# Optimization experiments

Measured on AMD Instinct MI355X. Metric: run time of the kernel, lower is better.

The kernel has to match this reference:

```python
import jax, jax.numpy as jnp
import numpy as np

EMBED = 1024
HEADS = 16
HEAD_DIM = EMBED // HEADS

def setup_inputs() -> dict:
    key = jax.random.key(0)
    ks = jax.random.split(key, 9)
    N, Q, K = 2, 2048, 2048
    queries = jax.random.normal(ks[0], (N, Q, EMBED), dtype=jnp.float32)
    keys_ = jax.random.normal(ks[1], (N, K, EMBED), dtype=jnp.float32)
    values = jax.random.normal(ks[2], (N, K, EMBED), dtype=jnp.float32)
    mask = jax.random.randint(ks[3], (N, 1, Q, K), 0, 2, dtype=jnp.int32)
    s = 1.0 / np.sqrt(EMBED)
    Wq = jax.random.normal(ks[4], (EMBED, EMBED), dtype=jnp.float32) * s
    Wk = jax.random.normal(ks[5], (EMBED, EMBED), dtype=jnp.float32) * s
    Wv = jax.random.normal(ks[6], (EMBED, EMBED), dtype=jnp.float32) * s
    Wo = jax.random.normal(ks[7], (EMBED, EMBED), dtype=jnp.float32) * s
    bo = jax.random.normal(ks[8], (EMBED,), dtype=jnp.float32) * s
    return {"queries": queries, "keys": keys_, "values": values, "mask": mask,
            "Wq": Wq, "Wk": Wk, "Wv": Wv, "Wo": Wo, "bo": bo}

def reference(queries, keys, values, mask, Wq, Wk, Wv, Wo, bo):
    N, Qlen, _ = queries.shape
    Klen = keys.shape[1]
    # Linear projections (torch Linear: x @ W.T), then split heads
    q = (queries @ Wq.T).reshape(N, Qlen, HEADS, HEAD_DIM)
    k = (keys @ Wk.T).reshape(N, Klen, HEADS, HEAD_DIM)
    v = (values @ Wv.T).reshape(N, Klen, HEADS, HEAD_DIM)
    energy = jnp.einsum('nqhd,nkhd->nhqk', q, k)  # [N,H,Q,K]
    energy = jnp.where(mask == 0, jnp.float32(-1e20), energy)
    # NOTE: original scales by sqrt(embed_size), not sqrt(head_dim)
    attention = jax.nn.softmax(energy / jnp.sqrt(jnp.float32(EMBED)), axis=3)
    out = jnp.einsum('nhqk,nkhd->nqhd', attention, v).reshape(N, Qlen, EMBED)
    return out @ Wo.T + bo
```

## Files before the change

### kernel.cpp

```cpp
#include <hip/hip_runtime.h>
#include <stdint.h>
#include <stddef.h>

typedef __attribute__((ext_vector_type(8)))  short bf16x8;
typedef __attribute__((ext_vector_type(2)))  float f32x2;
typedef __attribute__((ext_vector_type(4)))  float f32x4;
typedef __attribute__((ext_vector_type(16))) float f32x16;
typedef __attribute__((ext_vector_type(4)))  float float4v;
typedef __attribute__((ext_vector_type(4)))  int   int4v;

#define DEV static __device__ __forceinline__

static constexpr int EMBED  = 1024;
static constexpr int HEADS  = 16;
static constexpr int SEQ    = 2048;

DEV short f2bf(float f) {
  union { float f; unsigned u; } x; x.f = f;
  unsigned r = x.u + 0x7fffu + ((x.u >> 16) & 1u);
  return (short)(r >> 16);
}

DEV int cvtpk(float a, float b) {
  int r; asm("v_cvt_pk_bf16_f32 %0, %1, %2" : "=v"(r) : "v"(a), "v"(b)); return r;
}

DEV float fexp2(float x) { float r; asm("v_exp_f32 %0, %1" : "=v"(r) : "v"(x)); return r; }

#define MFMA16(a,b,c) __builtin_amdgcn_mfma_f32_16x16x32_bf16((a),(b),(c),0,0,0)
#define MFMA32(a,b,c) __builtin_amdgcn_mfma_f32_32x32x16_bf16((a),(b),(c),0,0,0)
#define GLDS(g,l) __builtin_amdgcn_global_load_lds( \
    (const __attribute__((address_space(1))) void*)(g), \
    (__attribute__((address_space(3))) void*)(l), 16, 0, 0)
#define SBAR0() __builtin_amdgcn_sched_barrier(0)
#define ZERO16 {0,0,0,0,0,0,0,0,0,0,0,0,0,0,0,0}
#define ROT3(x) ((x) == 2 ? 0 : (x) + 1)


struct CvtArgs { const float* src[7]; short* dst[7]; int n[7]; };

__global__ void cvt_bf16(CvtArgs a) {
  const int task = blockIdx.y;
  const int i = (blockIdx.x * 256 + threadIdx.x) * 8;
  if (i >= a.n[task]) return;
  const float4v* s = (const float4v*)(a.src[task] + i);
  float4v x = s[0], y = s[1];
  bf16x8 o;
  o[0] = f2bf(x[0]); o[1] = f2bf(x[1]); o[2] = f2bf(x[2]); o[3] = f2bf(x[3]);
  o[4] = f2bf(y[0]); o[5] = f2bf(y[1]); o[6] = f2bf(y[2]); o[7] = f2bf(y[3]);
  *(bf16x8*)(a.dst[task] + i) = o;
}

__global__ void maskpack(const int* __restrict__ m, unsigned long long* __restrict__ out) {
  const int gw = (blockIdx.x * 256 + threadIdx.x) >> 6;
  const int l  = threadIdx.x & 63;
  const int n = gw >> 16, kvblk = (gw >> 11) & 31, q = gw & 2047;
  int v = m[((size_t)n * SEQ + q) * SEQ + kvblk * 64 + l];
  unsigned long long b = __ballot(v != 0);
  if (l == 0) out[((size_t)n * 32 + kvblk) * SEQ + q] = b;
}

template<int MODE>
DEV void gemm_core(const int vv, const short* __restrict__ A, const short* __restrict__ B,
                   short* __restrict__ Cb, float* __restrict__ Cf,
                   const float* __restrict__ bias, short* As, short* Bs)
{
  const int t = threadIdx.x;
  const int l = t & 63, w = t >> 6;
  const int lr = l & 15, lh = l >> 4;
  const int m0 = (vv >> 3) * 128, n0 = (vv & 7) * 128;
  const int wr = w >> 1, wc = w & 1;
  f32x4 acc[4][4] = {};

  const int rA = t >> 2, cA = (t & 3) * 8;
  const short* gA  = A + (size_t)(m0 + rA) * 1024 + cA;
  const short* gA2 = gA + (size_t)64 * 1024;
  const short* gB  = B + (size_t)(n0 + rA) * 1024 + cA;
  const short* gB2 = gB + (size_t)64 * 1024;

  GLDS(gA,       As + w * 512);
  GLDS(gA2,      As + 2048 + w * 512);
  GLDS(gB,       Bs + w * 512);
  GLDS(gB2,      Bs + 2048 + w * 512);
  SBAR0();
  GLDS(gA + 32,  As + 4096 + w * 512);
  GLDS(gA2 + 32, As + 4096 + 2048 + w * 512);
  GLDS(gB + 32,  Bs + 4096 + w * 512);
  GLDS(gB2 + 32, Bs + 4096 + 2048 + w * 512);
  SBAR0();

  int cb = 0, sb = 2;
  #pragma unroll 1
  for (int it = 0; it < 32; ++it) {
    if (it < 31) { asm volatile("s_waitcnt vmcnt(4)" ::: "memory"); }
    else         { asm volatile("s_waitcnt vmcnt(0)" ::: "memory"); }
    SBAR0();
    __builtin_amdgcn_s_barrier();
    SBAR0();
    if (it < 30) {
      const int kt = (it + 2) * 32;
      GLDS(gA + kt,  As + sb * 4096 + w * 512);
      GLDS(gA2 + kt, As + sb * 4096 + 2048 + w * 512);
      GLDS(gB + kt,  Bs + sb * 4096 + w * 512);
      GLDS(gB2 + kt, Bs + sb * 4096 + 2048 + w * 512);
      SBAR0();
    }

    const short* as = As + cb * 4096;
    const short* bs = Bs + cb * 4096;
    bf16x8 af[4], bq[4];
    #pragma unroll
    for (int i = 0; i < 4; ++i)
      af[i] = *(const bf16x8*)&as[(wr * 64 + i * 16 + lr) * 32 + lh * 8];
    #pragma unroll
    for (int i = 0; i < 4; ++i)
      bq[i] = *(const bf16x8*)&bs[(wc * 64 + i * 16 + lr) * 32 + lh * 8];
    #pragma unroll
    for (int mi = 0; mi < 4; ++mi)
      #pragma unroll
      for (int ni = 0; ni < 4; ++ni)
        acc[mi][ni] = MFMA16(af[mi], bq[ni], acc[mi][ni]);

    SBAR0();
    cb = ROT3(cb); sb = ROT3(sb);
  }

  #pragma unroll
  for (int mi = 0; mi < 4; ++mi)
    #pragma unroll
    for (int ni = 0; ni < 4; ++ni)
      #pragma unroll
      for (int r = 0; r < 4; ++r) {
        const int m = m0 + wr * 64 + mi * 16 + lh * 4 + r;
        const int e = n0 + wc * 64 + ni * 16 + lr;
        const float v = acc[mi][ni][r];
        const int nb = m >> 11, s = m & 2047, hh = e >> 6, d = e & 63;
        if (MODE == 0) {
          Cb[(((size_t)(nb * HEADS + hh)) * SEQ + s) * 64 + d] = f2bf(v);
        } else if (MODE == 2) {
          Cb[(((size_t)(nb * HEADS + hh)) * SEQ + s) * 64 + (d ^ ((s & 7) << 3))] = f2bf(v);
        } else {
          Cb[(((size_t)(nb * HEADS + hh)) * 32 + (s >> 6)) * 4096 + d * 64 +
             ((s & 63) ^ ((d & 7) << 3))] = f2bf(v);
        }
      }
}

__global__ __launch_bounds__(256, 3)
void gemm_qkv(const short* __restrict__ Ab, const short* __restrict__ Bb,
              short* __restrict__ Qp, short* __restrict__ Kp, short* __restrict__ VTp)
{
  __shared__ short As[3][4096];
  __shared__ short Bs[3][4096];
  const int lin = blockIdx.x;
  const int s = lin >> 8, j = lin & 255;
  const int vv = (j & 7) * 32 + (j >> 3);
  const short* A = Ab + (size_t)s * 4194304;
  const short* B = Bb + (size_t)s * 1048576;
  if (s == 0)      gemm_core<0>(vv, A, B, Qp,  nullptr, nullptr, &As[0][0], &Bs[0][0]);
  else if (s == 1) gemm_core<2>(vv, A, B, Kp,  nullptr, nullptr, &As[0][0], &Bs[0][0]);
  else             gemm_core<3>(vv, A, B, VTp, nullptr, nullptr, &As[0][0], &Bs[0][0]);
}

__global__ __launch_bounds__(256, 2)
void gemm_out(const short* __restrict__ A, const short* __restrict__ B,
              float* __restrict__ Cf, const float* __restrict__ bias)
{
  __shared__ short AsArr[3][2048];
  __shared__ short BsArr[3][4096];
  short* As = &AsArr[0][0];
  short* Bs = &BsArr[0][0];
  const int lin = blockIdx.x;
  const int vv = (lin & 7) * 64 + (lin >> 3);
  const int t = threadIdx.x;
  const int l = t & 63, w = t >> 6;
  const int lr = l & 15, lh = l >> 4;
  const int m0 = (vv >> 3) * 64, n0 = (vv & 7) * 128;
  const int wr = w >> 1, wc = w & 1;
  f32x4 acc[2][4] = {};

  const int rA = t >> 2, cA = (t & 3) * 8;
  const short* gA  = A + (size_t)(m0 + rA) * 1024 + cA;
  const short* gB  = B + (size_t)(n0 + rA) * 1024 + cA;
  const short* gB2 = gB + (size_t)64 * 1024;

  GLDS(gA,       As + w * 512);
  GLDS(gB,       Bs + w * 512);
  GLDS(gB2,      Bs + 2048 + w * 512);
  SBAR0();
  GLDS(gA + 32,  As + 2048 + w * 512);
  GLDS(gB + 32,  Bs + 4096 + w * 512);
  GLDS(gB2 + 32, Bs + 4096 + 2048 + w * 512);
  SBAR0();

  int cb = 0, sb = 2;
  #pragma unroll 1
  for (int it = 0; it < 32; ++it) {
    if (it < 31) { asm volatile("s_waitcnt vmcnt(3)" ::: "memory"); }
    else         { asm volatile("s_waitcnt vmcnt(0)" ::: "memory"); }
    SBAR0();
    __builtin_amdgcn_s_barrier();
    SBAR0();
    if (it < 30) {
      const int kt = (it + 2) * 32;
      GLDS(gA + kt,  As + sb * 2048 + w * 512);
      GLDS(gB + kt,  Bs + sb * 4096 + w * 512);
      GLDS(gB2 + kt, Bs + sb * 4096 + 2048 + w * 512);
      SBAR0();
    }

    const short* as = As + cb * 2048;
    const short* bs = Bs + cb * 4096;
    bf16x8 af[2], bq[4];
    #pragma unroll
    for (int i = 0; i < 2; ++i)
      af[i] = *(const bf16x8*)&as[(wr * 32 + i * 16 + lr) * 32 + lh * 8];
    #pragma unroll
    for (int i = 0; i < 4; ++i)
      bq[i] = *(const bf16x8*)&bs[(wc * 64 + i * 16 + lr) * 32 + lh * 8];
    #pragma unroll
    for (int mi = 0; mi < 2; ++mi)
      #pragma unroll
      for (int ni = 0; ni < 4; ++ni)
        acc[mi][ni] = MFMA16(af[mi], bq[ni], acc[mi][ni]);

    SBAR0();
    cb = ROT3(cb); sb = ROT3(sb);
  }

  #pragma unroll
  for (int mi = 0; mi < 2; ++mi)
    #pragma unroll
    for (int ni = 0; ni < 4; ++ni)
      #pragma unroll
      for (int r = 0; r < 4; ++r) {
        const int m = m0 + wr * 32 + mi * 16 + lh * 4 + r;
        const int e = n0 + wc * 64 + ni * 16 + lr;
        Cf[(size_t)m * EMBED + e] = acc[mi][ni][r] + bias[e];
      }
}

__global__ __launch_bounds__(256, 2)
void attn256(const short* __restrict__ Qp, const short* __restrict__ Kp,
             const short* __restrict__ VTp, const unsigned long long* __restrict__ MbT,
             short* __restrict__ Aout)
{
  __shared__ short lds[2][8192];

  const int t = threadIdx.x, l = t & 63, w = t >> 6;
  const int lq = l & 31, hi = l >> 5;
  const int lin = blockIdx.x;
  const int vv = (lin & 7) * 64 + (lin >> 3);
  const int hl = vv >> 4, qb = vv & 15;
  const int n = hl >> 4, h = hl & 15;
  const int q0 = qb * 128;
  const int myq = q0 + w * 32 + lq;
  const size_t hb = (size_t)(n * HEADS + h) * SEQ * 64;
  const short* Qh = Qp + hb;
  const float SCL = 0.045084220027780106f;

  bf16x8 qf[4];
  #pragma unroll
  for (int ks = 0; ks < 4; ++ks)
    qf[ks] = *(const bf16x8*)(Qh + (size_t)myq * 64 + ks * 16 + hi * 8);

  const short ONE = (short)0x3F80;
  const bf16x8 onesv = {ONE, ONE, ONE, ONE, ONE, ONE, ONE, ONE};
  const f32x16 zerov = ZERO16;

  f32x16 acco[2] = { ZERO16, ZERO16 };
  f32x16 accl = ZERO16;

  const short* kgp = Kp + hb + w * 1024 + l * 8;
  const short* vgp = VTp + hb + w * 1024 + l * 8;
  const unsigned long long* mp = MbT + (size_t)n * (32 * SEQ) + myq;

  unsigned long long mw = *mp; mp += SEQ;
  {
    GLDS(kgp,       &lds[0][w * 1024]);
    GLDS(kgp + 512, &lds[0][w * 1024 + 512]);
    GLDS(vgp,       &lds[0][4096 + w * 1024]);
    GLDS(vgp + 512, &lds[0][4096 + w * 1024 + 512]);
    kgp += 4096; vgp += 4096;
  }

  #pragma unroll 1
  for (int tt = 0; tt < 32; ++tt) {
    unsigned long long mw_next = 0;
    if (tt < 31) {
      mw_next = *mp; mp += SEQ;
      SBAR0();
      const int nb = (tt + 1) & 1;
      GLDS(kgp,       &lds[nb][w * 1024]);
      GLDS(kgp + 512, &lds[nb][w * 1024 + 512]);
      GLDS(vgp,       &lds[nb][4096 + w * 1024]);
      GLDS(vgp + 512, &lds[nb][4096 + w * 1024 + 512]);
      kgp += 4096; vgp += 4096;
      asm volatile("s_waitcnt vmcnt(5)" ::: "memory");
      SBAR0();
    } else {
      asm volatile("s_waitcnt vmcnt(0)" ::: "memory");
      SBAR0();
    }
    __builtin_amdgcn_s_barrier();
    SBAR0();

    const short* Ks  = &lds[tt & 1][0];
    const short* VTs = &lds[tt & 1][4096];

    #pragma unroll
    for (int half = 0; half < 2; ++half) {
      f32x16 sacc;
      __builtin_amdgcn_s_setprio(1);
      #pragma unroll
      for (int ks = 0; ks < 4; ++ks) {
        const int d = ks * 16 + hi * 8;
        bf16x8 kf = *(const bf16x8*)&Ks[(half * 32 + lq) * 64 + (d ^ ((lq & 7) << 3))];
        sacc = MFMA32(kf, qf[ks], ks == 0 ? zerov : sacc);
      }
      __builtin_amdgcn_s_setprio(0);
      const unsigned mmw = ~(unsigned)(mw >> (half * 32 + hi * 4));
      float p[16];
      #pragma unroll
      for (int r = 0; r < 16; ++r) {
        const int idx = (r & 3) + 8 * (r >> 2);
        union { int i; float f; } b;
        b.i = __builtin_amdgcn_sbfe(mmw, idx, 1) & 0xC3480000;
        p[r] = fexp2(__builtin_fmaf(sacc[r], SCL, b.f));
      }
      bf16x8 pf[2];
      #pragma unroll
      for (int kb = 0; kb < 2; ++kb) {
        int x1 = cvtpk(p[kb * 8 + 0], p[kb * 8 + 1]);
        int y1 = cvtpk(p[kb * 8 + 4], p[kb * 8 + 5]);
        int x2 = cvtpk(p[kb * 8 + 2], p[kb * 8 + 3]);
        int y2 = cvtpk(p[kb * 8 + 6], p[kb * 8 + 7]);
        asm("v_permlane32_swap_b32 %0, %1" : "+v"(x1), "+v"(y1));
        asm("v_permlane32_swap_b32 %0, %1" : "+v"(x2), "+v"(y2));
        union { int w4[4]; bf16x8 v; } u;
        u.w4[0] = x1; u.w4[1] = x2; u.w4[2] = y1; u.w4[3] = y2;
        pf[kb] = u.v;
      }
      __builtin_amdgcn_s_setprio(1);
      accl = MFMA32(onesv, pf[0], accl);
      accl = MFMA32(onesv, pf[1], accl);
      #pragma unroll
      for (int dt = 0; dt < 2; ++dt) {
        const int d = dt * 32 + lq;
        #pragma unroll
        for (int kb = 0; kb < 2; ++kb) {
          const int kv = half * 32 + kb * 16 + hi * 8;
          bf16x8 vf = *(const bf16x8*)&VTs[d * 64 + (kv ^ ((d & 7) << 3))];
          acco[dt] = MFMA32(vf, pf[kb], acco[dt]);
        }
      }
      __builtin_amdgcn_s_setprio(0);
    }
    mw = mw_next;
    SBAR0();
    __builtin_amdgcn_s_barrier();
    SBAR0();
  }

  const float invs = 1.f / (accl[0] + 1e-30f);

  short* ot = &lds[0][0] + w * 2048;
  #pragma unroll
  for (int dt = 0; dt < 2; ++dt)
    #pragma unroll
    for (int r = 0; r < 16; ++r) {
      const int d = dt * 32 + (r & 3) + 8 * (r >> 2) + 4 * hi;
      ot[lq * 64 + (d ^ ((lq & 7) << 3))] = f2bf(acco[dt][r] * invs);
    }
  __syncthreads();

  const int qq = l >> 1, hb2 = l & 1;
  #pragma unroll
  for (int it = 0; it < 4; ++it) {
    const int didx = (hb2 * 32 + it * 8) ^ ((qq & 7) << 3);
    bf16x8 v = *(const bf16x8*)&ot[qq * 64 + didx];
    *(bf16x8*)&Aout[((size_t)(n * SEQ + q0 + w * 32 + qq)) * EMBED + h * 64 + hb2 * 32 + it * 8] = v;
  }
}

extern "C" void kernel_launch(void* const* d_in, const int* in_sizes, int n_in,
                              void* d_out, int out_size, void* d_ws, size_t ws_size,
                              hipStream_t stream) {
  (void)in_sizes; (void)n_in; (void)out_size;
  const float* queries = (const float*)d_in[0];
  const float* keys    = (const float*)d_in[1];
  const float* values  = (const float*)d_in[2];
  const int*   mask    = (const int*)d_in[3];
  const float* Wq      = (const float*)d_in[4];
  const float* Wk      = (const float*)d_in[5];
  const float* Wv      = (const float*)d_in[6];
  const float* Wo      = (const float*)d_in[7];
  const float* bo      = (const float*)d_in[8];

  const size_t NEED = (size_t)76 * 1024 * 1024;
  if (ws_size < NEED) return;

  char* ws = (char*)d_ws;
  short* qb   = (short*)(ws + 0);
  short* kb   = (short*)(ws + (8u << 20));
  short* vb   = (short*)(ws + (16u << 20));
  short* wqb  = (short*)(ws + (24u << 20));
  short* wkb  = (short*)(ws + (26u << 20));
  short* wvb  = (short*)(ws + (28u << 20));
  short* wob  = (short*)(ws + (30u << 20));
  unsigned long long* mbits = (unsigned long long*)(ws + (32u << 20));
  short* Qp   = (short*)(ws + (40u << 20));
  short* Kp   = (short*)(ws + (48u << 20));
  short* VTp  = (short*)(ws + (56u << 20));
  short* ao   = (short*)(ws + (64u << 20));

  const int NTOK = 2 * SEQ * EMBED;
  const int NW   = EMBED * EMBED;

  CvtArgs ca;
  ca.src[0] = queries; ca.dst[0] = qb;  ca.n[0] = NTOK;
  ca.src[1] = keys;    ca.dst[1] = kb;  ca.n[1] = NTOK;
  ca.src[2] = values;  ca.dst[2] = vb;  ca.n[2] = NTOK;
  ca.src[3] = Wq;      ca.dst[3] = wqb; ca.n[3] = NW;
  ca.src[4] = Wk;      ca.dst[4] = wkb; ca.n[4] = NW;
  ca.src[5] = Wv;      ca.dst[5] = wvb; ca.n[5] = NW;
  ca.src[6] = Wo;      ca.dst[6] = wob; ca.n[6] = NW;
  cvt_bf16<<<dim3(2048, 7), 256, 0, stream>>>(ca);

  maskpack<<<dim3(32768), 256, 0, stream>>>(mask, mbits);

  gemm_qkv<<<dim3(768), 256, 0, stream>>>(qb, wqb, Qp, Kp, VTp);

  attn256<<<dim3(512), 256, 0, stream>>>(Qp, Kp, VTp, mbits, ao);

  gemm_out<<<dim3(512), 256, 0, stream>>>(ao, wob, (float*)d_out, bo);
}
```

Before: 141.9 us.

## Fuse fp32-to-bf16 activation conversion into QKV GEMM loads

The QKV projection GEMM now reads fp32 activations straight from global memory into registers, packs them to bf16 and writes them to LDS itself. The separate conversion pass over queries, keys and values is dropped, so only the weights still go through the cvt kernel. This removes a full write and re-read of the bf16 activation copies. In exchange the A-operand path loses the async global-to-LDS load, reads twice as many bytes per tile, and needs an extra LDS barrier every iteration.

```diff
diff --git a/kernel.cpp b/kernel.cpp
--- a/kernel.cpp
+++ b/kernel.cpp
@@ -37,7 +37,7 @@
 #define ROT3(x) ((x) == 2 ? 0 : (x) + 1)
 
 
-struct CvtArgs { const float* src[7]; short* dst[7]; int n[7]; };
+struct CvtArgs { const float* src[4]; short* dst[4]; int n[4]; };
 
 __global__ void cvt_bf16(CvtArgs a) {
   const int task = blockIdx.y;
@@ -61,9 +61,8 @@
 }
 
 template<int MODE>
-DEV void gemm_core(const int vv, const short* __restrict__ A, const short* __restrict__ B,
-                   short* __restrict__ Cb, float* __restrict__ Cf,
-                   const float* __restrict__ bias, short* As, short* Bs)
+DEV void gemm_qkv_core(const int vv, const float* __restrict__ A, const short* __restrict__ B,
+                       short* __restrict__ Cb, short* As, short* Bs)
 {
   const int t = threadIdx.x;
   const int l = t & 63, w = t >> 6;
@@ -73,39 +72,71 @@
   f32x4 acc[4][4] = {};
 
   const int rA = t >> 2, cA = (t & 3) * 8;
-  const short* gA  = A + (size_t)(m0 + rA) * 1024 + cA;
-  const short* gA2 = gA + (size_t)64 * 1024;
+  const float* gA  = A + (size_t)(m0 + rA) * 1024 + cA;
+  const float* gA2 = gA + (size_t)64 * 1024;
   const short* gB  = B + (size_t)(n0 + rA) * 1024 + cA;
   const short* gB2 = gB + (size_t)64 * 1024;
 
-  GLDS(gA,       As + w * 512);
-  GLDS(gA2,      As + 2048 + w * 512);
+  short* wA  = As + t * 8;
+  short* wA2 = As + 2048 + t * 8;
+
+  float4v a0 = *(const float4v*)(gA);
+  float4v a1 = *(const float4v*)(gA + 4);
+  float4v a2 = *(const float4v*)(gA2);
+  float4v a3 = *(const float4v*)(gA2 + 4);
+  {
+    union { int w4[4]; bf16x8 v; } u1, u2;
+    u1.w4[0] = cvtpk(a0[0], a0[1]); u1.w4[1] = cvtpk(a0[2], a0[3]);
+    u1.w4[2] = cvtpk(a1[0], a1[1]); u1.w4[3] = cvtpk(a1[2], a1[3]);
+    u2.w4[0] = cvtpk(a2[0], a2[1]); u2.w4[1] = cvtpk(a2[2], a2[3]);
+    u2.w4[2] = cvtpk(a3[0], a3[1]); u2.w4[3] = cvtpk(a3[2], a3[3]);
+    *(bf16x8*)(wA)  = u1.v;
+    *(bf16x8*)(wA2) = u2.v;
+  }
+  SBAR0();
+  a0 = *(const float4v*)(gA + 32);
+  a1 = *(const float4v*)(gA + 36);
+  a2 = *(const float4v*)(gA2 + 32);
+  a3 = *(const float4v*)(gA2 + 36);
+  SBAR0();
   GLDS(gB,       Bs + w * 512);
   GLDS(gB2,      Bs + 2048 + w * 512);
-  SBAR0();
-  GLDS(gA + 32,  As + 4096 + w * 512);
-  GLDS(gA2 + 32, As + 4096 + 2048 + w * 512);
   GLDS(gB + 32,  Bs + 4096 + w * 512);
   GLDS(gB2 + 32, Bs + 4096 + 2048 + w * 512);
   SBAR0();
-
-  int cb = 0, sb = 2;
+  asm volatile("s_waitcnt vmcnt(0) lgkmcnt(0)" ::: "memory");
+  SBAR0();
+  __builtin_amdgcn_s_barrier();
+  SBAR0();
+
+  int cb = 0, sbA = 1, sbB = 2;
   #pragma unroll 1
   for (int it = 0; it < 32; ++it) {
-    if (it < 31) { asm volatile("s_waitcnt vmcnt(4)" ::: "memory"); }
-    else         { asm volatile("s_waitcnt vmcnt(0)" ::: "memory"); }
-    SBAR0();
-    __builtin_amdgcn_s_barrier();
-    SBAR0();
+    if (it > 0) {
+      if (it < 31) { asm volatile("s_waitcnt vmcnt(2)" ::: "memory"); }
+      else         { asm volatile("s_waitcnt vmcnt(0)" ::: "memory"); }
+      SBAR0();
+    }
+    if (it < 31) {
+      union { int w4[4]; bf16x8 v; } u1, u2;
+      u1.w4[0] = cvtpk(a0[0], a0[1]); u1.w4[1] = cvtpk(a0[2], a0[3]);
+      u1.w4[2] = cvtpk(a1[0], a1[1]); u1.w4[3] = cvtpk(a1[2], a1[3]);
+      u2.w4[0] = cvtpk(a2[0], a2[1]); u2.w4[1] = cvtpk(a2[2], a2[3]);
+      u2.w4[2] = cvtpk(a3[0], a3[1]); u2.w4[3] = cvtpk(a3[2], a3[3]);
+      *(bf16x8*)(wA  + sbA * 4096) = u1.v;
+      *(bf16x8*)(wA2 + sbA * 4096) = u2.v;
+      SBAR0();
+    }
     if (it < 30) {
       const int kt = (it + 2) * 32;
-      GLDS(gA + kt,  As + sb * 4096 + w * 512);
-      GLDS(gA2 + kt, As + sb * 4096 + 2048 + w * 512);
-      GLDS(gB + kt,  Bs + sb * 4096 + w * 512);
-      GLDS(gB2 + kt, Bs + sb * 4096 + 2048 + w * 512);
-      SBAR0();
-    }
-
+      a0 = *(const float4v*)(gA + kt);
+      a1 = *(const float4v*)(gA + kt + 4);
+      a2 = *(const float4v*)(gA2 + kt);
+      a3 = *(const float4v*)(gA2 + kt + 4);
+      GLDS(gB + kt,  Bs + sbB * 4096 + w * 512);
+      GLDS(gB2 + kt, Bs + sbB * 4096 + 2048 + w * 512);
+      SBAR0();
+    }
     const short* as = As + cb * 4096;
     const short* bs = Bs + cb * 4096;
     bf16x8 af[4], bq[4];
@@ -122,7 +153,11 @@
         acc[mi][ni] = MFMA16(af[mi], bq[ni], acc[mi][ni]);
 
     SBAR0();
-    cb = ROT3(cb); sb = ROT3(sb);
+    asm volatile("s_waitcnt lgkmcnt(0)" ::: "memory");
+    SBAR0();
+    __builtin_amdgcn_s_barrier();
+    SBAR0();
+    cb = ROT3(cb); sbA = ROT3(sbA); sbB = ROT3(sbB);
   }
 
   #pragma unroll
@@ -147,7 +182,8 @@
 }
 
 __global__ __launch_bounds__(256, 3)
-void gemm_qkv(const short* __restrict__ Ab, const short* __restrict__ Bb,
+void gemm_qkv(const float* __restrict__ Aq, const float* __restrict__ Ak,
+              const float* __restrict__ Av, const short* __restrict__ Bb,
               short* __restrict__ Qp, short* __restrict__ Kp, short* __restrict__ VTp)
 {
   __shared__ short As[3][4096];
@@ -155,11 +191,10 @@
   const int lin = blockIdx.x;
   const int s = lin >> 8, j = lin & 255;
   const int vv = (j & 7) * 32 + (j >> 3);
-  const short* A = Ab + (size_t)s * 4194304;
   const short* B = Bb + (size_t)s * 1048576;
-  if (s == 0)      gemm_core<0>(vv, A, B, Qp,  nullptr, nullptr, &As[0][0], &Bs[0][0]);
-  else if (s == 1) gemm_core<2>(vv, A, B, Kp,  nullptr, nullptr, &As[0][0], &Bs[0][0]);
-  else             gemm_core<3>(vv, A, B, VTp, nullptr, nullptr, &As[0][0], &Bs[0][0]);
+  if (s == 0)      gemm_qkv_core<0>(vv, Aq, B, Qp,  &As[0][0], &Bs[0][0]);
+  else if (s == 1) gemm_qkv_core<2>(vv, Ak, B, Kp,  &As[0][0], &Bs[0][0]);
+  else             gemm_qkv_core<3>(vv, Av, B, VTp, &As[0][0], &Bs[0][0]);
 }
 
 __global__ __launch_bounds__(256, 2)
@@ -401,12 +436,7 @@
   if (ws_size < NEED) return;
 
   char* ws = (char*)d_ws;
-  short* qb   = (short*)(ws + 0);
-  short* kb   = (short*)(ws + (8u << 20));
-  short* vb   = (short*)(ws + (16u << 20));
   short* wqb  = (short*)(ws + (24u << 20));
-  short* wkb  = (short*)(ws + (26u << 20));
-  short* wvb  = (short*)(ws + (28u << 20));
   short* wob  = (short*)(ws + (30u << 20));
   unsigned long long* mbits = (unsigned long long*)(ws + (32u << 20));
   short* Qp   = (short*)(ws + (40u << 20));
@@ -414,22 +444,18 @@
   short* VTp  = (short*)(ws + (56u << 20));
   short* ao   = (short*)(ws + (64u << 20));
 
-  const int NTOK = 2 * SEQ * EMBED;
-  const int NW   = EMBED * EMBED;
+  const int NW = EMBED * EMBED;
 
   CvtArgs ca;
-  ca.src[0] = queries; ca.dst[0] = qb;  ca.n[0] = NTOK;
-  ca.src[1] = keys;    ca.dst[1] = kb;  ca.n[1] = NTOK;
-  ca.src[2] = values;  ca.dst[2] = vb;  ca.n[2] = NTOK;
-  ca.src[3] = Wq;      ca.dst[3] = wqb; ca.n[3] = NW;
-  ca.src[4] = Wk;      ca.dst[4] = wkb; ca.n[4] = NW;
-  ca.src[5] = Wv;      ca.dst[5] = wvb; ca.n[5] = NW;
-  ca.src[6] = Wo;      ca.dst[6] = wob; ca.n[6] = NW;
-  cvt_bf16<<<dim3(2048, 7), 256, 0, stream>>>(ca);
+  ca.src[0] = Wq; ca.dst[0] = wqb;                         ca.n[0] = NW;
+  ca.src[1] = Wk; ca.dst[1] = (short*)(ws + (26u << 20));  ca.n[1] = NW;
+  ca.src[2] = Wv; ca.dst[2] = (short*)(ws + (28u << 20));  ca.n[2] = NW;
+  ca.src[3] = Wo; ca.dst[3] = wob;                         ca.n[3] = NW;
+  cvt_bf16<<<dim3(512, 4), 256, 0, stream>>>(ca);
 
   maskpack<<<dim3(32768), 256, 0, stream>>>(mask, mbits);
 
-  gemm_qkv<<<dim3(768), 256, 0, stream>>>(qb, wqb, Qp, Kp, VTp);
+  gemm_qkv<<<dim3(768), 256, 0, stream>>>(queries, keys, values, wqb, Qp, Kp, VTp);
 
   attn256<<<dim3(512), 256, 0, stream>>>(Qp, Kp, VTp, mbits, ao);
 
```

New measurement: 137.4 us. 3.1% less time.
